# Kernel optimization log

Hardware: AMD Instinct MI355X
Metric: run time of the kernel (lower is better)

Reference implementation:

```python
import jax, jax.numpy as jnp
import numpy as np

IN_FEATURES = 1024
OUT_FEATURES = 1024


def setup_inputs() -> dict:
    key = jax.random.key(0)
    k1, k2, k3, k4 = jax.random.split(key, 4)
    input = jax.random.normal(k1, (4096, IN_FEATURES), dtype=jnp.float32)
    mask = jax.random.uniform(k2, (512, 512, 512), dtype=jnp.float32)
    # nn.Linear params: weight [out, in], bias [out]
    bound = 1.0 / np.sqrt(IN_FEATURES)
    weight = jax.random.uniform(k3, (OUT_FEATURES, IN_FEATURES), dtype=jnp.float32,
                                minval=-bound, maxval=bound)
    bias = jax.random.uniform(k4, (OUT_FEATURES,), dtype=jnp.float32,
                              minval=-bound, maxval=bound)
    return {"input": input, "mask": mask, "weight": weight, "bias": bias}


def reference(input, mask, weight, bias):
    # LINEAR PASS: out = input @ W^T + b  -> [batch, out_features]
    out = jnp.einsum('bi,oi->bo', input, weight) + bias
    # scalar threshold = mean over batch of per-row sums
    threshold = out.sum(axis=1).mean()
    # The torch module extracts indices via host-side np.argwhere (data-dependent
    # shape). The jit-compatible device-side equivalent is the boolean mask of
    # elements exceeding the threshold; indices are recoverable via nonzero.
    hi_mask = mask > threshold
    return (out, hi_mask)
```

## Files before the change

kernel.cpp:

```cpp
#include <hip/hip_runtime.h>
#include <hip/hip_bf16.h>
#include <stdint.h>

#define M_ROWS 4096
#define N_OUT  1024
#define K_IN   1024
#define MASK_N 134217728

typedef __attribute__((ext_vector_type(8))) short bf16x8;
typedef __attribute__((ext_vector_type(4))) float f32x4;
typedef float f4v __attribute__((ext_vector_type(4)));

__device__ inline short f2bf(float f) {
    unsigned u = __float_as_uint(f);
    unsigned r = u + 0x7fffu + ((u >> 16) & 1u);
    return (short)(r >> 16);
}

__device__ inline float next_up(float f) {
    unsigned u = __float_as_uint(f);
    if (u == 0x80000000u || u == 0u) return __uint_as_float(0x00000001u);
    if (f > 0.0f) return __uint_as_float(u + 1u);
    return __uint_as_float(u - 1u);
}

__device__ inline void async16(const void* g, void* l) {
    __builtin_amdgcn_global_load_lds(
        (const __attribute__((address_space(1))) unsigned int*)g,
        (__attribute__((address_space(3))) unsigned int*)l, 16, 0, 0);
}

__global__ __launch_bounds__(256) void conv_colsum_kernel(
    const float* __restrict__ input, const float* __restrict__ weight,
    short* __restrict__ in_bf, short* __restrict__ w_bf,
    double* __restrict__ s_in, double* __restrict__ w_sum)
{
    int b = blockIdx.x;
    int t = threadIdx.x;
    const float* src; short* dst; double* sums; int row0;
    if (b < 256) { src = input;  dst = in_bf; sums = s_in;  row0 = b * 16; }
    else         { src = weight; dst = w_bf;  sums = w_sum; row0 = (b - 256) * 16; }

    const int kc = t >> 3;
    const int c  = (t >> 1) & 3;
    const int j0 = (t & 1) << 2;

    double a0 = 0, a1 = 0, a2 = 0, a3 = 0;
    for (int r = 0; r < 16; ++r) {
        int R = row0 + r;
        float4 v = *(const float4*)&src[(size_t)R * 1024 + 4 * t];
        int sc = c ^ ((R >> 1) & 3);
        short4 s4 = { f2bf(v.x), f2bf(v.y), f2bf(v.z), f2bf(v.w) };
        *(short4*)&dst[(size_t)R * 1024 + (kc << 5) + (sc << 3) + j0] = s4;
        a0 += (double)v.x; a1 += (double)v.y; a2 += (double)v.z; a3 += (double)v.w;
    }
    int c0 = 4 * t;
    atomicAdd(&sums[c0 + 0], a0);
    atomicAdd(&sums[c0 + 1], a1);
    atomicAdd(&sums[c0 + 2], a2);
    atomicAdd(&sums[c0 + 3], a3);
}

__global__ __launch_bounds__(1024) void threshold_kernel(
    const double* __restrict__ s_in, const double* __restrict__ w_sum,
    const float* __restrict__ bias, double* __restrict__ thr, float* __restrict__ cut)
{
    __shared__ double red[1024];
    int t = threadIdx.x;
    double v = s_in[t] * w_sum[t] * (1.0 / 4096.0) + (double)bias[t];
    red[t] = v;
    __syncthreads();
    for (int s = 512; s > 0; s >>= 1) {
        if (t < s) red[t] += red[t + s];
        __syncthreads();
    }
    if (t == 0) {
        double th = red[0];
        *thr = th;
        float f = (float)th;
        if ((double)f <= th) f = next_up(f);
        *cut = f;
    }
}

__global__ __launch_bounds__(256) void gemm_kernel(
    const short* __restrict__ Abf,
    const short* __restrict__ Wbf,
    const float* __restrict__ bias,
    float* __restrict__ C)
{
    __shared__ short As[128 * 32];
    __shared__ short Bs[128 * 32];

    const int tid  = threadIdx.x;
    const int wave = tid >> 6;
    const int lane = tid & 63;
    const int quad = lane >> 4;
    const int l16  = lane & 15;
    const int wr   = (wave >> 1) * 64;
    const int wc   = (wave & 1) * 64;

    const int tile_m = (blockIdx.x >> 3) * 128;
    const int tile_n = (blockIdx.x & 7) * 128;

    f32x4 acc[4][4];
    for (int i = 0; i < 4; ++i)
        for (int j = 0; j < 4; ++j)
            acc[i][j] = (f32x4){0.f, 0.f, 0.f, 0.f};

    const short* gA = Abf + (size_t)(tile_m + (tid >> 2)) * 1024 + ((tid & 3) << 3);
    const short* gB = Wbf + (size_t)(tile_n + (tid >> 2)) * 1024 + ((tid & 3) << 3);
    short* lA = &As[tid * 8];
    short* lB = &Bs[tid * 8];

    for (int k0 = 0; k0 < K_IN; k0 += 32) {
        async16(gA + k0,             lA);
        async16(gA + 64 * 1024 + k0, lA + 64 * 32);
        async16(gB + k0,             lB);
        async16(gB + 64 * 1024 + k0, lB + 64 * 32);
        __syncthreads();

        bf16x8 af[4], bfr[4];
        for (int i = 0; i < 4; ++i) {
            int ra = wr + i * 16 + l16;
            af[i]  = *(const bf16x8*)&As[ra * 32 + ((quad ^ ((ra >> 1) & 3)) << 3)];
            int rb = wc + i * 16 + l16;
            bfr[i] = *(const bf16x8*)&Bs[rb * 32 + ((quad ^ ((rb >> 1) & 3)) << 3)];
        }
        for (int i = 0; i < 4; ++i)
            for (int j = 0; j < 4; ++j)
                acc[i][j] = __builtin_amdgcn_mfma_f32_16x16x32_bf16(
                    af[i], bfr[j], acc[i][j], 0, 0, 0);
        __syncthreads();
    }

    for (int i = 0; i < 4; ++i) {
        for (int j = 0; j < 4; ++j) {
            int col = tile_n + wc + j * 16 + l16;
            float b = bias[col];
            for (int r = 0; r < 4; ++r) {
                int row = tile_m + wr + i * 16 + quad * 4 + r;
                C[(size_t)row * N_OUT + col] = acc[i][j][r] + b;
            }
        }
    }
}

__global__ __launch_bounds__(256) void mask_kernel(
    const f4v* __restrict__ mask, f4v* __restrict__ out,
    const float* __restrict__ cut_p, int n4)
{
    float cut = *cut_p;
    int i = blockIdx.x * blockDim.x + threadIdx.x;
    int stride = gridDim.x * blockDim.x;
    for (; i < n4; i += stride) {
        f4v m = __builtin_nontemporal_load(&mask[i]);
        f4v o;
        o.x = (m.x >= cut) ? 1.0f : 0.0f;
        o.y = (m.y >= cut) ? 1.0f : 0.0f;
        o.z = (m.z >= cut) ? 1.0f : 0.0f;
        o.w = (m.w >= cut) ? 1.0f : 0.0f;
        __builtin_nontemporal_store(o, &out[i]);
    }
}

extern "C" void kernel_launch(void* const* d_in, const int* in_sizes, int n_in,
                              void* d_out, int out_size, void* d_ws, size_t ws_size,
                              hipStream_t stream) {
    const float* input  = (const float*)d_in[0];
    const float* mask   = (const float*)d_in[1];
    const float* weight = (const float*)d_in[2];
    const float* bias   = (const float*)d_in[3];

    float* out = (float*)d_out;
    float* hi  = out + (size_t)M_ROWS * N_OUT;

    char* wsb = (char*)d_ws;
    double* s_in  = (double*)wsb;
    double* w_sum = (double*)(wsb + 8192);
    double* thr   = (double*)(wsb + 16384);
    float*  cut   = (float*)(wsb + 16384 + 8);
    short*  in_bf = (short*)(wsb + 32768);
    short*  w_bf  = (short*)(wsb + 32768 + (size_t)M_ROWS * K_IN * 2);

    hipMemsetAsync(d_ws, 0, 16384, stream);

    conv_colsum_kernel<<<320, 256, 0, stream>>>(input, weight, in_bf, w_bf, s_in, w_sum);
    threshold_kernel<<<1, 1024, 0, stream>>>(s_in, w_sum, bias, thr, cut);
    gemm_kernel<<<256, 256, 0, stream>>>(in_bf, w_bf, bias, out);
    mask_kernel<<<16384, 256, 0, stream>>>((const f4v*)mask, (f4v*)hi, cut, MASK_N / 4);
}
```

Before: 901.4 us.

## Merge GEMM and mask threshold into one launch to overlap compute and streaming

Fuses the mask comparison into the GEMM kernel launch: the first 256 blocks do the bf16 MFMA GEMM, and the remaining 16384 blocks each process eight float4 mask elements with all loads issued up front. The aim is to run the bandwidth-bound mask pass alongside the compute-bound GEMM and drop one kernel launch. The mask blocks share the GEMM's 256-thread shape and register/LDS footprint, which may lower occupancy for the streaming part, and block scheduling order decides how much overlap actually happens.

```diff
diff --git a/kernel.cpp b/kernel.cpp
--- a/kernel.cpp
+++ b/kernel.cpp
@@ -6,6 +6,7 @@
 #define N_OUT  1024
 #define K_IN   1024
 #define MASK_N 134217728
+#define MASK_BLOCKS 16384
 
 typedef __attribute__((ext_vector_type(8))) short bf16x8;
 typedef __attribute__((ext_vector_type(4))) float f32x4;
@@ -83,12 +84,35 @@
     }
 }
 
-__global__ __launch_bounds__(256) void gemm_kernel(
+__global__ __launch_bounds__(256) void gemm_mask_kernel(
     const short* __restrict__ Abf,
     const short* __restrict__ Wbf,
     const float* __restrict__ bias,
-    float* __restrict__ C)
+    float* __restrict__ C,
+    const f4v* __restrict__ mask,
+    f4v* __restrict__ hi,
+    const float* __restrict__ cut_p)
 {
+    if (blockIdx.x >= 256) {
+        float cut = *cut_p;
+        const size_t stride = (size_t)MASK_BLOCKS * 256;
+        size_t i0 = (size_t)(blockIdx.x - 256) * 256 + threadIdx.x;
+        f4v m[8];
+        #pragma unroll
+        for (int j = 0; j < 8; ++j)
+            m[j] = __builtin_nontemporal_load(&mask[i0 + (size_t)j * stride]);
+        #pragma unroll
+        for (int j = 0; j < 8; ++j) {
+            f4v o;
+            o.x = (m[j].x >= cut) ? 1.0f : 0.0f;
+            o.y = (m[j].y >= cut) ? 1.0f : 0.0f;
+            o.z = (m[j].z >= cut) ? 1.0f : 0.0f;
+            o.w = (m[j].w >= cut) ? 1.0f : 0.0f;
+            __builtin_nontemporal_store(o, &hi[i0 + (size_t)j * stride]);
+        }
+        return;
+    }
+
     __shared__ short As[128 * 32];
     __shared__ short Bs[128 * 32];
 
@@ -146,24 +170,6 @@
     }
 }
 
-__global__ __launch_bounds__(256) void mask_kernel(
-    const f4v* __restrict__ mask, f4v* __restrict__ out,
-    const float* __restrict__ cut_p, int n4)
-{
-    float cut = *cut_p;
-    int i = blockIdx.x * blockDim.x + threadIdx.x;
-    int stride = gridDim.x * blockDim.x;
-    for (; i < n4; i += stride) {
-        f4v m = __builtin_nontemporal_load(&mask[i]);
-        f4v o;
-        o.x = (m.x >= cut) ? 1.0f : 0.0f;
-        o.y = (m.y >= cut) ? 1.0f : 0.0f;
-        o.z = (m.z >= cut) ? 1.0f : 0.0f;
-        o.w = (m.w >= cut) ? 1.0f : 0.0f;
-        __builtin_nontemporal_store(o, &out[i]);
-    }
-}
-
 extern "C" void kernel_launch(void* const* d_in, const int* in_sizes, int n_in,
                               void* d_out, int out_size, void* d_ws, size_t ws_size,
                               hipStream_t stream) {
@@ -187,6 +193,6 @@
 
     conv_colsum_kernel<<<320, 256, 0, stream>>>(input, weight, in_bf, w_bf, s_in, w_sum);
     threshold_kernel<<<1, 1024, 0, stream>>>(s_in, w_sum, bias, thr, cut);
-    gemm_kernel<<<256, 256, 0, stream>>>(in_bf, w_bf, bias, out);
-    mask_kernel<<<16384, 256, 0, stream>>>((const f4v*)mask, (f4v*)hi, cut, MASK_N / 4);
+    gemm_mask_kernel<<<256 + MASK_BLOCKS, 256, 0, stream>>>(
+        in_bf, w_bf, bias, out, (const f4v*)mask, (f4v*)hi, cut);
 }
```

Result: no change. 901.2 us (-0.0%).
